# Optimization experiments

Hardware: AMD Instinct MI355X
Metric: run time of the kernel (lower is better)

## Reference

```python
import jax, jax.numpy as jnp
import numpy as np

NEG = -9e10


def _gat_layer(h_in, adj_mask, W, a, alpha, concat):
    # h_in: [N, Fin], W: [Fin, Fout], a: [2*Fout, 1]
    h = h_in @ W                                  # [N, Fout]
    Fout = W.shape[1]
    a1 = a[:Fout, 0]                              # [Fout]
    a2 = a[Fout:, 0]                              # [Fout]
    # e[i,j] = leakyrelu(h_i . a1 + h_j . a2)  (decomposed repeat+cat score)
    s1 = h @ a1                                   # [N]
    s2 = h @ a2                                   # [N]
    e = jax.nn.leaky_relu(s1[:, None] + s2[None, :], negative_slope=alpha)  # [N, N]
    e = jnp.where(adj_mask, e, NEG)
    att = jax.nn.softmax(e, axis=1)               # [N, N]
    h_prime = att @ h                             # [N, Fout]
    return jax.nn.elu(h_prime) if concat else h_prime


def setup_inputs() -> dict:
    key = jax.random.key(0)
    ks = jax.random.split(key, 6)
    N, nfeat, nhid, nheads, nout = 4096, 512, 64, 8, 56
    x = jax.random.normal(ks[0], (N, nfeat), dtype=jnp.float32)
    adj = jax.random.randint(ks[1], (N, N), 0, 2, dtype=jnp.int32)
    Ws = jax.random.normal(ks[2], (nheads, nfeat, nhid), dtype=jnp.float32) * 0.05
    As = jax.random.normal(ks[3], (nheads, 2 * nhid, 1), dtype=jnp.float32) * 0.05
    W_out = jax.random.normal(ks[4], (nhid, nout), dtype=jnp.float32) * 0.05
    a_out = jax.random.normal(ks[5], (2 * nout, 1), dtype=jnp.float32) * 0.05
    return {"x": x, "adj": adj, "Ws": Ws, "As": As, "W_out": W_out, "a_out": a_out}


def reference(x, adj, Ws, As, W_out, a_out):
    alpha = 0.2
    nheads = Ws.shape[0]
    adj_mask = adj > 0
    # dropout is identity in eval mode
    heads = jax.vmap(lambda W, a: _gat_layer(x, adj_mask, W, a, alpha, True))(Ws, As)
    z = jnp.sum(heads, axis=0) / nheads           # [N, nhid] (heads averaged, per source)
    out = _gat_layer(z, adj_mask, W_out, a_out, alpha, False)
    out = jax.nn.elu(out)                         # [N, 56]
    return jax.nn.softmax(out, axis=1)
```

## Files before the change

kernel.cpp:

```cpp
#include <hip/hip_runtime.h>
#include <hip/hip_bf16.h>
#include <math.h>


#define GN 4096
#define GNH 8
#define LOG2E 1.4426950408889634f

typedef __bf16 bf16x8 __attribute__((ext_vector_type(8)));
typedef float f32x4 __attribute__((ext_vector_type(4)));

#if defined(__has_builtin)
#if __has_builtin(__builtin_amdgcn_exp2f)
#define FAST_EXP2(x) __builtin_amdgcn_exp2f(x)
#endif
#if __has_builtin(__builtin_amdgcn_perm)
#define FAST_PERM(a, b, s) __builtin_amdgcn_perm((a), (b), (s))
#endif
#endif
#ifndef FAST_EXP2
#define FAST_EXP2(x) __expf((x)*0.6931471805599453f)
#endif
#ifndef FAST_PERM
__device__ inline unsigned FAST_PERM(unsigned a, unsigned b, unsigned) {
    return (a & 0xFFFF0000u) | (b >> 16);
}
#endif

__device__ inline unsigned hi_pack2(float w0, float w1) {
    unsigned u0 = __float_as_uint(w0) + 0x8000u;
    unsigned u1 = __float_as_uint(w1) + 0x8000u;
    return FAST_PERM(u1, u0, 0x07060302u);
}

__global__ __launch_bounds__(256) void prep(const int* __restrict__ adj,
                                            const float* __restrict__ x,
                                            const float* __restrict__ Ws,
                                            unsigned long long* __restrict__ adjb,
                                            unsigned short* __restrict__ xh,
                                            unsigned short* __restrict__ wth) {
    const int b = blockIdx.x;
    const int tid = threadIdx.x;
    if (b < 16384) {
        const int wv = tid >> 6, lane = tid & 63;
        const size_t ebase = ((size_t)b * 4 + wv) * 256;
        unsigned long long m[4];
        #pragma unroll
        for (int e = 0; e < 4; ++e)
            m[e] = __ballot(adj[ebase + e * 64 + lane] > 0);
        if (lane == 0) {
            #pragma unroll
            for (int e = 0; e < 4; ++e) adjb[(ebase >> 6) + e] = m[e];
        }
    } else if (b < 17408) {
        int gid = (b - 16384) * 256 + tid;
        int i = gid >> 6, c64 = gid & 63;
        const float* xp = x + (size_t)i * 512 + c64 * 8;
        float4 a = *(const float4*)xp;
        float4 v = *(const float4*)(xp + 4);
        unsigned hp[4];
        hp[0] = hi_pack2(a.x, a.y);
        hp[1] = hi_pack2(a.z, a.w);
        hp[2] = hi_pack2(v.x, v.y);
        hp[3] = hi_pack2(v.z, v.w);
        int il = i & 63, kt = c64 >> 3, c = c64 & 7;
        size_t base = ((size_t)(i >> 6) * 8 + kt) * 4096 + il * 64 + ((c ^ (il & 7)) * 8);
        *(uint4*)&xh[base] = *(uint4*)hp;
    } else {
        __shared__ float t[64][65];
        int b2 = b - 17408;
        int head = b2 >> 3, k0 = (b2 & 7) * 64;
        #pragma unroll
        for (int it = 0; it < 4; ++it) {
            int e = (tid + it * 256) * 4;
            int kl = e >> 6, f4 = e & 63;
            float4 v = *(const float4*)&Ws[((size_t)head * 512 + k0 + kl) * 64 + f4];
            t[f4 + 0][kl] = v.x; t[f4 + 1][kl] = v.y;
            t[f4 + 2][kl] = v.z; t[f4 + 3][kl] = v.w;
        }
        __syncthreads();
        int f = tid >> 2;
        #pragma unroll
        for (int p = 0; p < 2; ++p) {
            int c = (tid & 3) * 2 + p;
            unsigned hp[4];
            #pragma unroll
            for (int pp = 0; pp < 4; ++pp)
                hp[pp] = hi_pack2(t[f][c * 8 + 2 * pp], t[f][c * 8 + 2 * pp + 1]);
            size_t base = (size_t)b2 * 4096 + f * 64 + ((c ^ (f & 7)) * 8);
            *(uint4*)&wth[base] = *(uint4*)hp;
        }
    }
}

__global__ __launch_bounds__(256) void gemm_fused(const unsigned short* __restrict__ xh,
                                                  const unsigned short* __restrict__ wth,
                                                  const float* __restrict__ As,
                                                  unsigned short* __restrict__ imgh,
                                                  float* __restrict__ s1L,
                                                  float* __restrict__ s2L) {
    __shared__ __align__(16) unsigned short lds[2][2][4096];
    const int tid = threadIdx.x;
    const int head = blockIdx.x;
    const int itile = blockIdx.y;
    const int i0 = itile * 64;
    const unsigned short* srcs[2] = {xh + (size_t)itile * 8 * 4096,
                                     wth + (size_t)head * 8 * 4096};
    const int lane = tid & 63, wv_ = tid >> 6;
    const int mi = (wv_ & 1) * 32, fi = (wv_ >> 1) * 32;
    const int row = lane & 15, quad = lane >> 4;
    f32x4 acc[2][2] = {};

    #define GSTAGE(buf, kt)                                                                \
        do {                                                                               \
            _Pragma("unroll")                                                              \
            for (int q_ = 0; q_ < 2; ++q_) {                                               \
                const unsigned short* s_ = srcs[q_] + (size_t)(kt) * 4096;                 \
                _Pragma("unroll")                                                          \
                for (int c_ = 0; c_ < 2; ++c_)                                             \
                    __builtin_amdgcn_global_load_lds(                                      \
                        (const __attribute__((address_space(1))) unsigned int*)(s_ + c_ * 2048 + tid * 8), \
                        (__attribute__((address_space(3))) unsigned int*)&lds[buf][q_][c_ * 2048 + tid * 8], \
                        16, 0, 0);                                                         \
            }                                                                              \
        } while (0)

    GSTAGE(0, 0);
    for (int kt = 0; kt < 8; ++kt) {
        __syncthreads();
        const int cur = kt & 1;
        if (kt + 1 < 8) GSTAGE(cur ^ 1, kt + 1);
        #pragma unroll
        for (int ks = 0; ks < 2; ++ks) {
            bf16x8 ah[2], bh[2];
            #pragma unroll
            for (int t = 0; t < 2; ++t) {
                const int m_ = mi + t * 16 + row;
                const int offa = m_ * 64 + (((ks * 4 + quad) ^ (m_ & 7)) * 8);
                ah[t] = *(const bf16x8*)&lds[cur][0][offa];
                const int f_ = fi + t * 16 + row;
                const int offb = f_ * 64 + (((ks * 4 + quad) ^ (f_ & 7)) * 8);
                bh[t] = *(const bf16x8*)&lds[cur][1][offb];
            }
            #pragma unroll
            for (int mt = 0; mt < 2; ++mt)
                #pragma unroll
                for (int nt = 0; nt < 2; ++nt)
                    acc[mt][nt] = __builtin_amdgcn_mfma_f32_16x16x32_bf16(ah[mt], bh[nt], acc[mt][nt], 0, 0, 0);
        }
    }
    #undef GSTAGE
    __syncthreads();
    float* ht = (float*)&lds[0][0][0];
    #pragma unroll
    for (int mt = 0; mt < 2; ++mt)
        #pragma unroll
        for (int nt = 0; nt < 2; ++nt)
            #pragma unroll
            for (int r = 0; r < 4; ++r)
                ht[(mi + mt * 16 + quad * 4 + r) * 68 + fi + nt * 16 + row] = acc[mt][nt][r];
    __syncthreads();
    {
        const int rrow = tid >> 2, seg = (tid & 3) * 16;
        const float* ah = As + head * 128;
        float p1 = 0.f, p2 = 0.f;
        #pragma unroll
        for (int c = 0; c < 16; ++c) {
            float v = ht[rrow * 68 + seg + c];
            p1 += v * ah[seg + c];
            p2 += v * ah[64 + seg + c];
        }
        p1 += __shfl_xor(p1, 1); p1 += __shfl_xor(p1, 2);
        p2 += __shfl_xor(p2, 1); p2 += __shfl_xor(p2, 2);
        if ((tid & 3) == 0) {
            s1L[head * GN + i0 + rrow] = p1 * LOG2E;
            s2L[head * GN + i0 + rrow] = p2 * LOG2E;
        }
    }
    {
        const int f = tid >> 2;
        size_t base = ((size_t)head * 64 + itile) * 4096 + (size_t)f * 64;
        #pragma unroll
        for (int p = 0; p < 2; ++p) {
            int c = (tid & 3) * 2 + p;
            unsigned hp[4];
            #pragma unroll
            for (int pp = 0; pp < 4; ++pp)
                hp[pp] = hi_pack2(ht[(c * 8 + 2 * pp) * 68 + f], ht[(c * 8 + 2 * pp + 1) * 68 + f]);
            int off = (c ^ (f & 7)) * 8;
            *(uint4*)&imgh[base + off] = *(uint4*)hp;
        }
    }
}

template <int NCHUNK>
__global__ __launch_bounds__(256, 4) void attn10(const unsigned short* __restrict__ imgh,
                                                 const float* __restrict__ s1g,
                                                 const float* __restrict__ s2g,
                                                 const unsigned long long* __restrict__ adjb,
                                                 float* __restrict__ pO,
                                                 float* __restrict__ pd) {
    __shared__ __align__(16) unsigned short hb[2][4096];
    const int tid = threadIdx.x;
    const int lane = tid & 63, wv = tid >> 6;
    const int row = lane & 15, quad = lane >> 4;
    const int head = blockIdx.y / NCHUNK;
    const int chunk = blockIdx.y % NCHUNK;
    const int i0 = blockIdx.x * 64;
    const int jb = chunk * (GN / NCHUNK);
    const int njt = (GN / NCHUNK) / 64;
    const int jt0 = jb >> 6;
    const unsigned short* ih = imgh + (size_t)head * (64 * GN);
    const float* s2h = s2g + head * GN;
    const int gr = i0 + wv * 16 + row;
    const float s1v = s1g[head * GN + gr];
    const unsigned long long* adjr = adjb + (size_t)gr * 64 + jt0;

    f32x4 acc[4] = {};
    float den = 0.f;

    #define STAGE(buf, T)                                                                  \
        do {                                                                               \
            const unsigned short* gh_ = ih + (size_t)(T) * 4096;                           \
            _Pragma("unroll")                                                              \
            for (int c_ = 0; c_ < 2; ++c_)                                                 \
                __builtin_amdgcn_global_load_lds(                                          \
                    (const __attribute__((address_space(1))) unsigned int*)(gh_ + c_ * 2048 + tid * 8), \
                    (__attribute__((address_space(3))) unsigned int*)&hb[buf][c_ * 2048 + tid * 8],     \
                    16, 0, 0);                                                             \
        } while (0)

    STAGE(0, jt0);
    for (int jt = 0; jt < njt; ++jt) {
        __syncthreads();
        const int cur = jt & 1;
        const int j0 = jb + jt * 64;
        const unsigned long long wd = adjr[jt];
        float4 sa0 = *(const float4*)&s2h[j0 + quad * 8];
        float4 sb0 = *(const float4*)&s2h[j0 + quad * 8 + 4];
        float4 sa1 = *(const float4*)&s2h[j0 + 32 + quad * 8];
        float4 sb1 = *(const float4*)&s2h[j0 + 32 + quad * 8 + 4];
        if (jt + 1 < njt) STAGE(cur ^ 1, jt0 + jt + 1);
        #pragma unroll
        for (int ks = 0; ks < 2; ++ks) {
            const int kb = ks * 32 + quad * 8;
            const float s2v[8] = {ks ? sa1.x : sa0.x, ks ? sa1.y : sa0.y,
                                  ks ? sa1.z : sa0.z, ks ? sa1.w : sa0.w,
                                  ks ? sb1.x : sb0.x, ks ? sb1.y : sb0.y,
                                  ks ? sb1.z : sb0.z, ks ? sb1.w : sb0.w};
            const unsigned bits = (unsigned)(wd >> kb) & 0xFFu;
            union { unsigned u[4]; bf16x8 v; } hfr;
            #pragma unroll
            for (int p = 0; p < 4; ++p) {
                float m0 = (float)((bits >> (2 * p)) & 1u);
                float m1 = (float)((bits >> (2 * p + 1)) & 1u);
                float t0 = s1v + s2v[2 * p];
                float t1 = s1v + s2v[2 * p + 1];
                float w0 = FAST_EXP2(fmaxf(t0, 0.2f * t0)) * m0;
                float w1 = FAST_EXP2(fmaxf(t1, 0.2f * t1)) * m1;
                unsigned u0 = __float_as_uint(w0) + 0x8000u;
                unsigned u1 = __float_as_uint(w1) + 0x8000u;
                den += __uint_as_float(u0 & 0xFFFF0000u) + __uint_as_float(u1 & 0xFFFF0000u);
                hfr.u[p] = FAST_PERM(u1, u0, 0x07060302u);
            }
            #pragma unroll
            for (int nt = 0; nt < 4; ++nt) {
                const int f = nt * 16 + row;
                const int off = f * 64 + (((ks * 4 + quad) ^ (f & 7)) * 8);
                bf16x8 bh = *(const bf16x8*)&hb[cur][off];
                acc[nt] = __builtin_amdgcn_mfma_f32_16x16x32_bf16(hfr.v, bh, acc[nt], 0, 0, 0);
            }
        }
    }
    #undef STAGE
    den += __shfl_xor(den, 16);
    den += __shfl_xor(den, 32);
    float* o = pO + (size_t)blockIdx.y * (GN * 64);
    #pragma unroll
    for (int r = 0; r < 4; ++r) {
        const int grow = i0 + wv * 16 + quad * 4 + r;
        #pragma unroll
        for (int nt = 0; nt < 4; ++nt)
            o[(size_t)grow * 64 + nt * 16 + row] = acc[nt][r];
    }
    if (lane < 16) pd[blockIdx.y * GN + i0 + wv * 16 + lane] = den;
}

__global__ __launch_bounds__(256) void mid(const float* __restrict__ pO,
                                           const float* __restrict__ pd,
                                           const float* __restrict__ Wo,
                                           const float* __restrict__ ao,
                                           unsigned short* __restrict__ img2h,
                                           float* __restrict__ s1bL,
                                           float* __restrict__ s2bL) {
    __shared__ __align__(16) float zt[16][68];
    __shared__ float Wl[64 * 57];
    __shared__ float invd[8][16];
    const int tid = threadIdx.x;
    const int i0 = blockIdx.x * 16;
    for (int idx = tid; idx < 64 * 56; idx += 256) {
        int k = idx / 56, c = idx - k * 56;
        Wl[k * 57 + c] = Wo[idx];
    }
    if (tid < 128) {
        int hd = tid >> 4, r = tid & 15;
        invd[hd][r] = 1.f / (pd[(2 * hd) * GN + i0 + r] + pd[(2 * hd + 1) * GN + i0 + r]);
    }
    __syncthreads();
    #pragma unroll
    for (int it = 0; it < 4; ++it) {
        int e = it * 256 + tid;
        int r = e >> 6, f = e & 63;
        size_t base = (size_t)(i0 + r) * 64 + f;
        float s = 0.f;
        #pragma unroll
        for (int hd = 0; hd < GNH; ++hd) {
            float o = pO[(size_t)(2 * hd) * (GN * 64) + base] +
                      pO[(size_t)(2 * hd + 1) * (GN * 64) + base];
            float v = o * invd[hd][r];
            s += v > 0.f ? v : FAST_EXP2(v * LOG2E) - 1.f;
        }
        zt[r][f] = s * 0.125f;
    }
    __syncthreads();
    const int rrow = tid >> 4, cseg = (tid & 15) * 4;
    float hreg[4] = {0.f, 0.f, 0.f, 0.f};
    for (int k0 = 0; k0 < 64; k0 += 4) {
        float4 zv = *(const float4*)&zt[rrow][k0];
        #pragma unroll
        for (int c = 0; c < 4; ++c) {
            int col = cseg + c;
            if (col < 56)
                hreg[c] += zv.x * Wl[k0 * 57 + col] + zv.y * Wl[(k0 + 1) * 57 + col] +
                           zv.z * Wl[(k0 + 2) * 57 + col] + zv.w * Wl[(k0 + 3) * 57 + col];
        }
    }
    {
        float p1 = 0.f, p2 = 0.f;
        #pragma unroll
        for (int c = 0; c < 4; ++c) {
            int col = cseg + c;
            if (col < 56) {
                p1 += hreg[c] * ao[col];
                p2 += hreg[c] * ao[56 + col];
            }
        }
        p1 += __shfl_xor(p1, 1); p1 += __shfl_xor(p1, 2);
        p1 += __shfl_xor(p1, 4); p1 += __shfl_xor(p1, 8);
        p2 += __shfl_xor(p2, 1); p2 += __shfl_xor(p2, 2);
        p2 += __shfl_xor(p2, 4); p2 += __shfl_xor(p2, 8);
        if ((tid & 15) == 0) {
            s1bL[i0 + rrow] = p1 * LOG2E;
            s2bL[i0 + rrow] = p2 * LOG2E;
        }
    }
    __syncthreads();
    #pragma unroll
    for (int c = 0; c < 4; ++c) zt[rrow][cseg + c] = (cseg + c < 56) ? hreg[c] : 0.f;
    __syncthreads();
    if (tid < 128) {
        const int jt = i0 >> 6;
        const int cbase = (i0 & 63) >> 3;
        const int f = tid >> 1, c = cbase + (tid & 1);
        const int lr = (tid & 1) * 8;
        unsigned hp[4];
        #pragma unroll
        for (int pp = 0; pp < 4; ++pp)
            hp[pp] = hi_pack2(zt[lr + 2 * pp][f], zt[lr + 2 * pp + 1][f]);
        size_t base = (size_t)jt * 4096 + f * 64 + ((c ^ (f & 7)) * 8);
        *(uint4*)&img2h[base] = *(uint4*)hp;
    }
}

__global__ __launch_bounds__(256) void fink2(const float* __restrict__ pO,
                                             const float* __restrict__ pd,
                                             float* __restrict__ out) {
    const int lane = threadIdx.x & 63;
    const int w = threadIdx.x >> 6;
    const int i = blockIdx.x * 4 + w;
    float o = 0.f, d = 0.f;
    #pragma unroll
    for (int c = 0; c < 16; ++c) d += pd[c * GN + i];
    if (lane < 56) {
        #pragma unroll
        for (int c = 0; c < 16; ++c) o += pO[(size_t)c * (GN * 64) + (size_t)i * 64 + lane];
    }
    float v = -1e30f;
    if (lane < 56) {
        float t = o / d;
        v = t > 0.f ? t : expm1f(t);
    }
    float m = v;
    #pragma unroll
    for (int off = 32; off; off >>= 1) m = fmaxf(m, __shfl_down(m, off));
    m = __shfl(m, 0);
    float p = (lane < 56) ? __expf(v - m) : 0.f;
    float s = p;
    #pragma unroll
    for (int off = 32; off; off >>= 1) s += __shfl_down(s, off);
    s = __shfl(s, 0);
    if (lane < 56) out[(size_t)i * 56 + lane] = p / s;
}

extern "C" void kernel_launch(void* const* d_in, const int* in_sizes, int n_in,
                              void* d_out, int out_size, void* d_ws, size_t ws_size,
                              hipStream_t stream) {
    const float* x    = (const float*)d_in[0];
    const int*   adj  = (const int*)d_in[1];
    const float* Ws   = (const float*)d_in[2];
    const float* As   = (const float*)d_in[3];
    const float* Wo   = (const float*)d_in[4];
    const float* ao   = (const float*)d_in[5];
    float* out = (float*)d_out;

    char* ws = (char*)d_ws;
    unsigned long long* adjb = (unsigned long long*)(ws + 0);
    unsigned short* img1h = (unsigned short*)(ws + 2097152);
    float* pO    = (float*)(ws + 6291456);
    unsigned short* x_hi = (unsigned short*)(ws + 6291456);
    float* pd    = (float*)(ws + 23068672);
    float* s1L   = (float*)(ws + 23330816);
    float* s2L   = (float*)(ws + 23461888);
    float* s1bL  = (float*)(ws + 23592960);
    float* s2bL  = (float*)(ws + 23609344);
    unsigned short* img2h = (unsigned short*)(ws + 23625728);
    unsigned short* WT_hi = (unsigned short*)(ws + 24150016);

    prep<<<17472, 256, 0, stream>>>(adj, x, Ws, adjb, x_hi, WT_hi);
    gemm_fused<<<dim3(8, 64), 256, 0, stream>>>(x_hi, WT_hi, As, img1h, s1L, s2L);
    attn10<2><<<dim3(64, 16), 256, 0, stream>>>(img1h, s1L, s2L, adjb, pO, pd);
    mid<<<256, 256, 0, stream>>>(pO, pd, Wo, ao, img2h, s1bL, s2bL);
    attn10<16><<<dim3(64, 16), 256, 0, stream>>>(img2h, s1bL, s2bL, adjb, pO, pd);
    fink2<<<1024, 256, 0, stream>>>(pO, pd, out);
}
```

Before: 205.8 us.

## Factor leaky-relu exp into per-node exponentials to remove per-edge exp2

Rewrites exp(leakyrelu(s1+s2)) as max(exp(0.8*s1)*exp(s2), exp(0.2*s2)) scaled by exp(0.2*s1), precomputing per-node exponentials in the producer kernels. Each attention weight then costs a multiply and a max instead of an exp2, which lowers transcendental work in the N×N inner loop. The constant per-row factor cancels in the softmax. The trade-offs are twice the bytes loaded per j for the float2 tables, and a risk of overflow or underflow because no max is subtracted before exponentiating.

```diff
diff --git a/kernel.cpp b/kernel.cpp
--- a/kernel.cpp
+++ b/kernel.cpp
@@ -97,8 +97,8 @@
                                                   const unsigned short* __restrict__ wth,
                                                   const float* __restrict__ As,
                                                   unsigned short* __restrict__ imgh,
-                                                  float* __restrict__ s1L,
-                                                  float* __restrict__ s2L) {
+                                                  float* __restrict__ rL,
+                                                  float2* __restrict__ ebL) {
     __shared__ __align__(16) unsigned short lds[2][2][4096];
     const int tid = threadIdx.x;
     const int head = blockIdx.x;
@@ -173,8 +173,12 @@
         p1 += __shfl_xor(p1, 1); p1 += __shfl_xor(p1, 2);
         p2 += __shfl_xor(p2, 1); p2 += __shfl_xor(p2, 2);
         if ((tid & 3) == 0) {
-            s1L[head * GN + i0 + rrow] = p1 * LOG2E;
-            s2L[head * GN + i0 + rrow] = p2 * LOG2E;
+            const int gi = i0 + rrow;
+            rL[head * GN + gi] = FAST_EXP2(0.8f * p1 * LOG2E);
+            float2 e;
+            e.x = FAST_EXP2(p2 * LOG2E);
+            e.y = FAST_EXP2(0.2f * p2 * LOG2E);
+            ebL[head * GN + gi] = e;
         }
     }
     {
@@ -195,8 +199,8 @@
 
 template <int NCHUNK>
 __global__ __launch_bounds__(256, 4) void attn10(const unsigned short* __restrict__ imgh,
-                                                 const float* __restrict__ s1g,
-                                                 const float* __restrict__ s2g,
+                                                 const float* __restrict__ rg,
+                                                 const float2* __restrict__ ebg,
                                                  const unsigned long long* __restrict__ adjb,
                                                  float* __restrict__ pO,
                                                  float* __restrict__ pd) {
@@ -211,9 +215,9 @@
     const int njt = (GN / NCHUNK) / 64;
     const int jt0 = jb >> 6;
     const unsigned short* ih = imgh + (size_t)head * (64 * GN);
-    const float* s2h = s2g + head * GN;
+    const float2* ebh = ebg + (size_t)head * GN;
     const int gr = i0 + wv * 16 + row;
-    const float s1v = s1g[head * GN + gr];
+    const float rv = rg[head * GN + gr];
     const unsigned long long* adjr = adjb + (size_t)gr * 64 + jt0;
 
     f32x4 acc[4] = {};
@@ -236,28 +240,25 @@
         const int cur = jt & 1;
         const int j0 = jb + jt * 64;
         const unsigned long long wd = adjr[jt];
-        float4 sa0 = *(const float4*)&s2h[j0 + quad * 8];
-        float4 sb0 = *(const float4*)&s2h[j0 + quad * 8 + 4];
-        float4 sa1 = *(const float4*)&s2h[j0 + 32 + quad * 8];
-        float4 sb1 = *(const float4*)&s2h[j0 + 32 + quad * 8 + 4];
+        const float4* ep0 = (const float4*)(ebh + j0 + quad * 8);
+        const float4* ep1 = (const float4*)(ebh + j0 + 32 + quad * 8);
+        const float4 f00 = ep0[0], f01 = ep0[1], f02 = ep0[2], f03 = ep0[3];
+        const float4 f10 = ep1[0], f11 = ep1[1], f12 = ep1[2], f13 = ep1[3];
         if (jt + 1 < njt) STAGE(cur ^ 1, jt0 + jt + 1);
         #pragma unroll
         for (int ks = 0; ks < 2; ++ks) {
             const int kb = ks * 32 + quad * 8;
-            const float s2v[8] = {ks ? sa1.x : sa0.x, ks ? sa1.y : sa0.y,
-                                  ks ? sa1.z : sa0.z, ks ? sa1.w : sa0.w,
-                                  ks ? sb1.x : sb0.x, ks ? sb1.y : sb0.y,
-                                  ks ? sb1.z : sb0.z, ks ? sb1.w : sb0.w};
             const unsigned bits = (unsigned)(wd >> kb) & 0xFFu;
+            const float4 e4[4] = {ks ? f10 : f00, ks ? f11 : f01,
+                                  ks ? f12 : f02, ks ? f13 : f03};
             union { unsigned u[4]; bf16x8 v; } hfr;
             #pragma unroll
             for (int p = 0; p < 4; ++p) {
-                float m0 = (float)((bits >> (2 * p)) & 1u);
-                float m1 = (float)((bits >> (2 * p + 1)) & 1u);
-                float t0 = s1v + s2v[2 * p];
-                float t1 = s1v + s2v[2 * p + 1];
-                float w0 = FAST_EXP2(fmaxf(t0, 0.2f * t0)) * m0;
-                float w1 = FAST_EXP2(fmaxf(t1, 0.2f * t1)) * m1;
+                const float4 e = e4[p];
+                const float m0 = (float)((bits >> (2 * p)) & 1u);
+                const float m1 = (float)((bits >> (2 * p + 1)) & 1u);
+                const float w0 = fmaxf(rv * e.x, e.y) * m0;
+                const float w1 = fmaxf(rv * e.z, e.w) * m1;
                 unsigned u0 = __float_as_uint(w0) + 0x8000u;
                 unsigned u1 = __float_as_uint(w1) + 0x8000u;
                 den += __uint_as_float(u0 & 0xFFFF0000u) + __uint_as_float(u1 & 0xFFFF0000u);
@@ -291,8 +292,8 @@
                                            const float* __restrict__ Wo,
                                            const float* __restrict__ ao,
                                            unsigned short* __restrict__ img2h,
-                                           float* __restrict__ s1bL,
-                                           float* __restrict__ s2bL) {
+                                           float* __restrict__ rbL,
+                                           float2* __restrict__ eb2L) {
     __shared__ __align__(16) float zt[16][68];
     __shared__ float Wl[64 * 57];
     __shared__ float invd[8][16];
@@ -350,8 +351,11 @@
         p2 += __shfl_xor(p2, 1); p2 += __shfl_xor(p2, 2);
         p2 += __shfl_xor(p2, 4); p2 += __shfl_xor(p2, 8);
         if ((tid & 15) == 0) {
-            s1bL[i0 + rrow] = p1 * LOG2E;
-            s2bL[i0 + rrow] = p2 * LOG2E;
+            rbL[i0 + rrow] = FAST_EXP2(0.8f * p1 * LOG2E);
+            float2 e;
+            e.x = FAST_EXP2(p2 * LOG2E);
+            e.y = FAST_EXP2(0.2f * p2 * LOG2E);
+            eb2L[i0 + rrow] = e;
         }
     }
     __syncthreads();
@@ -419,17 +423,17 @@
     float* pO    = (float*)(ws + 6291456);
     unsigned short* x_hi = (unsigned short*)(ws + 6291456);
     float* pd    = (float*)(ws + 23068672);
-    float* s1L   = (float*)(ws + 23330816);
-    float* s2L   = (float*)(ws + 23461888);
-    float* s1bL  = (float*)(ws + 23592960);
-    float* s2bL  = (float*)(ws + 23609344);
-    unsigned short* img2h = (unsigned short*)(ws + 23625728);
-    unsigned short* WT_hi = (unsigned short*)(ws + 24150016);
+    float* rL    = (float*)(ws + 23330816);
+    float2* ebL  = (float2*)(ws + 23461888);
+    float* rbL   = (float*)(ws + 23724032);
+    float2* eb2L = (float2*)(ws + 23740416);
+    unsigned short* img2h = (unsigned short*)(ws + 23773184);
+    unsigned short* WT_hi = (unsigned short*)(ws + 24297472);
 
     prep<<<17472, 256, 0, stream>>>(adj, x, Ws, adjb, x_hi, WT_hi);
-    gemm_fused<<<dim3(8, 64), 256, 0, stream>>>(x_hi, WT_hi, As, img1h, s1L, s2L);
-    attn10<2><<<dim3(64, 16), 256, 0, stream>>>(img1h, s1L, s2L, adjb, pO, pd);
-    mid<<<256, 256, 0, stream>>>(pO, pd, Wo, ao, img2h, s1bL, s2bL);
-    attn10<16><<<dim3(64, 16), 256, 0, stream>>>(img2h, s1bL, s2bL, adjb, pO, pd);
+    gemm_fused<<<dim3(8, 64), 256, 0, stream>>>(x_hi, WT_hi, As, img1h, rL, ebL);
+    attn10<2><<<dim3(64, 16), 256, 0, stream>>>(img1h, rL, ebL, adjb, pO, pd);
+    mid<<<256, 256, 0, stream>>>(pO, pd, Wo, ao, img2h, rbL, eb2L);
+    attn10<16><<<dim3(64, 16), 256, 0, stream>>>(img2h, rbL, eb2L, adjb, pO, pd);
     fink2<<<1024, 256, 0, stream>>>(pO, pd, out);
 }
```

After: 215.5 us. 1.05x slower.
